# Kernel tuning notes

Hardware: AMD Instinct MI355X
Metric: run time of the kernel (lower is better)

The kernel has to match this reference:

```python
import jax, jax.numpy as jnp
import numpy as np

NUM_ROWS = 4096      # out_features
GROUP_COUNT = 32
GROUP_SIZE = 128     # in_features = GROUP_COUNT * GROUP_SIZE = 4096
CODEBOOK_SIZE = 16   # 4-bit codes


def setup_inputs() -> dict:
    key = jax.random.key(0)
    k1, k2, k3, k4 = jax.random.split(key, 4)
    x = jax.random.normal(k1, (2, 1024, GROUP_COUNT * GROUP_SIZE), dtype=jnp.float32)
    codebooks = jax.random.normal(k2, (NUM_ROWS, GROUP_COUNT, CODEBOOK_SIZE), dtype=jnp.float32)
    codes = jax.random.randint(k3, (NUM_ROWS, GROUP_COUNT, GROUP_SIZE), 0, CODEBOOK_SIZE, dtype=jnp.int32)
    bias = jax.random.normal(k4, (NUM_ROWS,), dtype=jnp.float32)
    return {"x": x, "codebooks": codebooks, "codes": codes, "bias": bias}


def _dequantize_weight(codes, codebooks):
    # codes: [R, G, S] int indices into last dim of codebooks [R, G, B]
    R, G, S = codes.shape
    W_hat = jnp.take_along_axis(codebooks, codes, axis=2)  # [R, G, S]
    return W_hat.reshape(R, G * S)  # [out_features, in_features]


def reference(x, codebooks, codes, bias):
    W = _dequantize_weight(codes, codebooks)           # [out, in]
    out = jnp.einsum("bsi,oi->bso", x, W) + bias       # F.linear
    return out
```

## Files before the change

kernel.cpp:

```cpp
#include <hip/hip_runtime.h>
#include <hip/hip_bf16.h>
#include <stdint.h>


#define M_DIM 2048
#define N_DIM 4096
#define K_DIM 4096

typedef __attribute__((ext_vector_type(4))) int i32x4;

__device__ __forceinline__ void async_load16(const void* g, void* l) {
    __builtin_amdgcn_global_load_lds(
        (const __attribute__((address_space(1))) uint32_t*)(uintptr_t)g,
        (__attribute__((address_space(3))) uint32_t*)(uint32_t)(uintptr_t)l,
        16, 0, 0);
}

__device__ __forceinline__ uint32_t pack4(int a, int b, int c, int d) {
    return (uint32_t)(a & 255) | ((uint32_t)(b & 255) << 8) |
           ((uint32_t)(c & 255) << 16) | ((uint32_t)(d & 255) << 24);
}

__device__ __forceinline__ int q8(float v, float inv) {
    return (int)rintf(v * inv);
}

__global__ __launch_bounds__(256) void prepass_q8(
    const float* __restrict__ cb,
    const int* __restrict__ codes,
    const float* __restrict__ x,
    uint32_t* __restrict__ wq,
    uint32_t* __restrict__ xq,
    float* __restrict__ sw,
    float* __restrict__ sx)
{
    __shared__ float scb[512];
    __shared__ float red[256];
    const int b = blockIdx.x, t = threadIdx.x;
    if (b < N_DIM) {
        const int o = b;
        const float c0 = cb[(size_t)o * 512 + t];
        const float c1 = cb[(size_t)o * 512 + 256 + t];
        scb[t] = c0; scb[t + 256] = c1;
        red[t] = fmaxf(fabsf(c0), fabsf(c1));
        __syncthreads();
        for (int s = 128; s > 0; s >>= 1) {
            if (t < s) red[t] = fmaxf(red[t], red[t + s]);
            __syncthreads();
        }
        const float amax = fmaxf(red[0], 1e-20f);
        const float inv = 127.0f / amax;
        if (t == 0) sw[o] = amax / 127.0f;
        const int* crow = codes + (size_t)o * K_DIM;
        uint32_t* orow = wq + (size_t)o * 1024;
#pragma unroll
        for (int i = 0; i < 4; ++i) {
            const int d = t + i * 256;
            const int4 c = *(const int4*)(crow + d * 4);
            const float* g = scb + (d >> 5) * 16;
            orow[d] = pack4(q8(g[c.x], inv), q8(g[c.y], inv),
                            q8(g[c.z], inv), q8(g[c.w], inv));
        }
    } else {
        const int m = b - N_DIM;
        const float* row = x + (size_t)m * K_DIM;
        float4 v[4];
        float am = 0.f;
#pragma unroll
        for (int i = 0; i < 4; ++i) {
            v[i] = *(const float4*)(row + (size_t)(t + i * 256) * 4);
            am = fmaxf(am, fmaxf(fmaxf(fabsf(v[i].x), fabsf(v[i].y)),
                                 fmaxf(fabsf(v[i].z), fabsf(v[i].w))));
        }
        red[t] = am;
        __syncthreads();
        for (int s = 128; s > 0; s >>= 1) {
            if (t < s) red[t] = fmaxf(red[t], red[t + s]);
            __syncthreads();
        }
        const float amax = fmaxf(red[0], 1e-20f);
        const float inv = 127.0f / amax;
        if (t == 0) sx[m] = amax / 127.0f;
        uint32_t* orow = xq + (size_t)m * 1024;
#pragma unroll
        for (int i = 0; i < 4; ++i)
            orow[t + i * 256] = pack4(q8(v[i].x, inv), q8(v[i].y, inv),
                                      q8(v[i].z, inv), q8(v[i].w, inv));
    }
}


__device__ __forceinline__ void compute_tile(
    const unsigned char* As, const unsigned char* Bs,
    const int wm, const int wn, const int l15, const int fs,
    i32x4 acc[8][4])
{
    i32x4 af[8], bf[4];
#pragma unroll
    for (int i = 0; i < 8; ++i)
        af[i] = *(const i32x4*)(As + (wm + i * 16 + l15) * 128 + fs);
#pragma unroll
    for (int i = 0; i < 4; ++i)
        bf[i] = *(const i32x4*)(Bs + (wn + i * 16 + l15) * 128 + fs);
#pragma unroll
    for (int mi = 0; mi < 8; ++mi)
#pragma unroll
        for (int ni = 0; ni < 4; ++ni)
            acc[mi][ni] = __builtin_amdgcn_mfma_i32_16x16x64_i8(
                af[mi], bf[ni], acc[mi][ni], 0, 0, 0);
}

__global__ __launch_bounds__(512, 2) void gemm_i8(
    const unsigned char* __restrict__ A,
    const unsigned char* __restrict__ B,
    const float* __restrict__ sx,
    const float* __restrict__ sw,
    const float* __restrict__ bias,
    float* __restrict__ C)
{
    __shared__ __align__(16) unsigned char smem[98304];
    unsigned char* As0 = smem;
    unsigned char* Bs0 = smem + 32768;
    unsigned char* As1 = smem + 49152;
    unsigned char* Bs1 = smem + 81920;

    const int tid  = threadIdx.x;
    const int w    = tid >> 6;
    const int lane = tid & 63;
    const int l15  = lane & 15;
    const int quad = lane >> 4;
    const int m0   = blockIdx.y * 256;
    const int n0   = blockIdx.x * 128;
    const int wk   = w >> 2;
    const int wm   = ((w >> 1) & 1) * 128;
    const int wn   = (w & 1) * 64;

    const int r8 = lane >> 3;
    const int sc = (lane & 7) ^ r8;
    const unsigned char* gA = A + (size_t)(m0 + w * 8 + r8) * K_DIM + sc * 16;
    const unsigned char* gB = B + (size_t)(n0 + w * 8 + r8) * K_DIM + sc * 16;

    const int fs = (((wk << 2) + quad) ^ (l15 & 7)) * 16;

    auto stage = [&](unsigned char* As, unsigned char* Bs, int k) {
        async_load16(gA + k,                        As +         w * 1024);
        async_load16(gA + k + (size_t)64  * K_DIM,  As + 8192  + w * 1024);
        async_load16(gA + k + (size_t)128 * K_DIM,  As + 16384 + w * 1024);
        async_load16(gA + k + (size_t)192 * K_DIM,  As + 24576 + w * 1024);
        async_load16(gB + k,                        Bs +         w * 1024);
        async_load16(gB + k + (size_t)64  * K_DIM,  Bs + 8192  + w * 1024);
    };

    i32x4 acc[8][4] = {};

    stage(As0, Bs0, 0);
    for (int k0 = 0; k0 < K_DIM; k0 += 256) {
        stage(As1, Bs1, k0 + 128);
        asm volatile("s_waitcnt vmcnt(6)" ::: "memory");
        __builtin_amdgcn_s_barrier();
        asm volatile("" ::: "memory");
        compute_tile(As0, Bs0, wm, wn, l15, fs, acc);
        asm volatile("s_waitcnt lgkmcnt(0)" ::: "memory");
        __builtin_amdgcn_sched_barrier(0);
        __builtin_amdgcn_s_barrier();

        if (k0 + 256 < K_DIM) {
            stage(As0, Bs0, k0 + 256);
            asm volatile("s_waitcnt vmcnt(6)" ::: "memory");
        } else {
            asm volatile("s_waitcnt vmcnt(0)" ::: "memory");
        }
        __builtin_amdgcn_s_barrier();
        asm volatile("" ::: "memory");
        compute_tile(As1, Bs1, wm, wn, l15, fs, acc);
        asm volatile("s_waitcnt lgkmcnt(0)" ::: "memory");
        __builtin_amdgcn_sched_barrier(0);
        __builtin_amdgcn_s_barrier();
    }

    i32x4* red = (i32x4*)smem;
    if (w == 4 || w == 5) {
        i32x4* dst = red + (w & 1) * 2048;
#pragma unroll
        for (int mi = 0; mi < 8; ++mi)
#pragma unroll
            for (int ni = 0; ni < 4; ++ni)
                dst[(mi * 4 + ni) * 64 + lane] = acc[mi][ni];
    }
    __syncthreads();
    if (w == 0 || w == 1) {
        const i32x4* src = red + (w & 1) * 2048;
#pragma unroll
        for (int mi = 0; mi < 8; ++mi)
#pragma unroll
            for (int ni = 0; ni < 4; ++ni) {
                const i32x4 v = src[(mi * 4 + ni) * 64 + lane];
                acc[mi][ni] = acc[mi][ni] + v;
            }
    }
    __syncthreads();
    if (w == 6 || w == 7) {
        i32x4* dst = red + (w & 1) * 2048;
#pragma unroll
        for (int mi = 0; mi < 8; ++mi)
#pragma unroll
            for (int ni = 0; ni < 4; ++ni)
                dst[(mi * 4 + ni) * 64 + lane] = acc[mi][ni];
    }
    __syncthreads();
    if (w == 2 || w == 3) {
        const i32x4* src = red + (w & 1) * 2048;
#pragma unroll
        for (int mi = 0; mi < 8; ++mi)
#pragma unroll
            for (int ni = 0; ni < 4; ++ni) {
                const i32x4 v = src[(mi * 4 + ni) * 64 + lane];
                acc[mi][ni] = acc[mi][ni] + v;
            }
    }

    if (w < 4) {
        float swv[4], bv[4];
#pragma unroll
        for (int ni = 0; ni < 4; ++ni) {
            const int col = n0 + wn + ni * 16 + l15;
            swv[ni] = sw[col];
            bv[ni]  = bias[col];
        }
#pragma unroll
        for (int mi = 0; mi < 8; ++mi) {
            float sxr[4];
#pragma unroll
            for (int r = 0; r < 4; ++r)
                sxr[r] = sx[m0 + wm + mi * 16 + quad * 4 + r];
#pragma unroll
            for (int ni = 0; ni < 4; ++ni) {
                const int col = n0 + wn + ni * 16 + l15;
                float* cp = C + (size_t)(m0 + wm + mi * 16 + quad * 4) * N_DIM + col;
#pragma unroll
                for (int r = 0; r < 4; ++r)
                    cp[(size_t)r * N_DIM] =
                        (float)acc[mi][ni][r] * (sxr[r] * swv[ni]) + bv[ni];
            }
        }
    }
}

__global__ __launch_bounds__(256) void naive_kernel(
    const float* __restrict__ x, const float* __restrict__ cb,
    const int* __restrict__ codes, const float* __restrict__ bias,
    float* __restrict__ out)
{
    const size_t idx = (size_t)blockIdx.x * 256 + threadIdx.x;
    const int n = (int)(idx & 4095);
    const int m = (int)(idx >> 12);
    const float* xr = x + (size_t)m * K_DIM;
    float s = bias[n];
    for (int g = 0; g < 32; ++g) {
        const float* cbr = cb + ((size_t)n * 32 + g) * 16;
        const int* cr = codes + ((size_t)n * 32 + g) * 128;
        const float* xg = xr + g * 128;
        for (int ss = 0; ss < 128; ++ss) s += xg[ss] * cbr[cr[ss]];
    }
    out[idx] = s;
}

extern "C" void kernel_launch(void* const* d_in, const int* in_sizes, int n_in,
                              void* d_out, int out_size, void* d_ws, size_t ws_size,
                              hipStream_t stream) {
    const float* x     = (const float*)d_in[0];
    const float* cb    = (const float*)d_in[1];
    const int*   codes = (const int*)d_in[2];
    const float* bias  = (const float*)d_in[3];
    float* out = (float*)d_out;

    const size_t szW = (size_t)N_DIM * K_DIM;
    const size_t szX = (size_t)M_DIM * K_DIM;
    const size_t need = szW + szX + (N_DIM + M_DIM) * sizeof(float);

    if (ws_size >= need) {
        unsigned char* Wq = (unsigned char*)d_ws;
        unsigned char* Xq = Wq + szW;
        float* sw = (float*)(Xq + szX);
        float* sx = sw + N_DIM;
        prepass_q8<<<dim3(N_DIM + M_DIM), dim3(256), 0, stream>>>(
            cb, codes, x, (uint32_t*)Wq, (uint32_t*)Xq, sw, sx);
        gemm_i8<<<dim3(N_DIM / 128, M_DIM / 256), dim3(512), 0, stream>>>(
            Xq, Wq, sx, sw, bias, out);
    } else {
        naive_kernel<<<dim3((M_DIM * N_DIM) / 256), dim3(256), 0, stream>>>(x, cb, codes, bias, out);
    }
}
```

Measured before the change: 173.8 us.

## Triple-buffer LDS and interleave async prefetch with half-tile MFMA phases

Replaces the double-buffered main loop with a three-stage LDS ring, prefetching two K-tiles ahead. Each K-tile is split into two MFMA halves: the A prefetch is issued between the first fragment loads and the first half, and the B prefetch before the second half. Barriers and s_setprio raise wave priority around the MFMA bursts. The goal is to hide global-load latency and spread the LDS-write traffic across the compute instead of issuing it in one burst. The cost is extra LDS (144KB), more barriers per tile, and tighter wait-count bookkeeping.

```diff
diff --git a/kernel.cpp b/kernel.cpp
--- a/kernel.cpp
+++ b/kernel.cpp
@@ -90,24 +90,60 @@
 }
 
 
-__device__ __forceinline__ void compute_tile(
-    const unsigned char* As, const unsigned char* Bs,
-    const int wm, const int wn, const int l15, const int fs,
-    i32x4 acc[8][4])
+template <bool STAGE, int VM>
+__device__ __forceinline__ void ktile(
+    const unsigned char* As_c, const unsigned char* Bs_c,
+    unsigned char* As_p, unsigned char* Bs_p, int kpre,
+    const unsigned char* gA, const unsigned char* gB,
+    int wm, int wn, int l15, int fs, int w, i32x4 acc[8][4])
 {
-    i32x4 af[8], bf[4];
-#pragma unroll
-    for (int i = 0; i < 8; ++i)
-        af[i] = *(const i32x4*)(As + (wm + i * 16 + l15) * 128 + fs);
+    i32x4 af[4], bf[4];
 #pragma unroll
     for (int i = 0; i < 4; ++i)
-        bf[i] = *(const i32x4*)(Bs + (wn + i * 16 + l15) * 128 + fs);
-#pragma unroll
-    for (int mi = 0; mi < 8; ++mi)
+        af[i] = *(const i32x4*)(As_c + (wm + i * 16 + l15) * 128 + fs);
+#pragma unroll
+    for (int i = 0; i < 4; ++i)
+        bf[i] = *(const i32x4*)(Bs_c + (wn + i * 16 + l15) * 128 + fs);
+    if (STAGE) {
+        async_load16(gA + kpre,                         As_p +         w * 1024);
+        async_load16(gA + kpre + (size_t)64  * K_DIM,   As_p + 8192  + w * 1024);
+        async_load16(gA + kpre + (size_t)128 * K_DIM,   As_p + 16384 + w * 1024);
+        async_load16(gA + kpre + (size_t)192 * K_DIM,   As_p + 24576 + w * 1024);
+    }
+    asm volatile("" ::: "memory");
+    __builtin_amdgcn_s_barrier();
+    __builtin_amdgcn_s_setprio(1);
+#pragma unroll
+    for (int mi = 0; mi < 4; ++mi)
 #pragma unroll
         for (int ni = 0; ni < 4; ++ni)
             acc[mi][ni] = __builtin_amdgcn_mfma_i32_16x16x64_i8(
                 af[mi], bf[ni], acc[mi][ni], 0, 0, 0);
+    __builtin_amdgcn_s_setprio(0);
+    asm volatile("" ::: "memory");
+    __builtin_amdgcn_s_barrier();
+
+#pragma unroll
+    for (int i = 0; i < 4; ++i)
+        af[i] = *(const i32x4*)(As_c + (wm + 64 + i * 16 + l15) * 128 + fs);
+    if (STAGE) {
+        async_load16(gB + kpre,                         Bs_p +        w * 1024);
+        async_load16(gB + kpre + (size_t)64 * K_DIM,    Bs_p + 8192 + w * 1024);
+    }
+    asm volatile("" ::: "memory");
+    __builtin_amdgcn_s_barrier();
+    __builtin_amdgcn_s_setprio(1);
+#pragma unroll
+    for (int mi = 0; mi < 4; ++mi)
+#pragma unroll
+        for (int ni = 0; ni < 4; ++ni)
+            acc[4 + mi][ni] = __builtin_amdgcn_mfma_i32_16x16x64_i8(
+                af[mi], bf[ni], acc[4 + mi][ni], 0, 0, 0);
+    __builtin_amdgcn_s_setprio(0);
+    if (VM == 6)      asm volatile("s_waitcnt vmcnt(6)" ::: "memory");
+    else if (VM == 0) asm volatile("s_waitcnt vmcnt(0)" ::: "memory");
+    asm volatile("" ::: "memory");
+    __builtin_amdgcn_s_barrier();
 }
 
 __global__ __launch_bounds__(512, 2) void gemm_i8(
@@ -118,11 +154,13 @@
     const float* __restrict__ bias,
     float* __restrict__ C)
 {
-    __shared__ __align__(16) unsigned char smem[98304];
+    __shared__ __align__(16) unsigned char smem[147456];
     unsigned char* As0 = smem;
     unsigned char* Bs0 = smem + 32768;
     unsigned char* As1 = smem + 49152;
     unsigned char* Bs1 = smem + 81920;
+    unsigned char* As2 = smem + 98304;
+    unsigned char* Bs2 = smem + 131072;
 
     const int tid  = threadIdx.x;
     const int w    = tid >> 6;
@@ -142,41 +180,37 @@
 
     const int fs = (((wk << 2) + quad) ^ (l15 & 7)) * 16;
 
-    auto stage = [&](unsigned char* As, unsigned char* Bs, int k) {
-        async_load16(gA + k,                        As +         w * 1024);
-        async_load16(gA + k + (size_t)64  * K_DIM,  As + 8192  + w * 1024);
-        async_load16(gA + k + (size_t)128 * K_DIM,  As + 16384 + w * 1024);
-        async_load16(gA + k + (size_t)192 * K_DIM,  As + 24576 + w * 1024);
-        async_load16(gB + k,                        Bs +         w * 1024);
-        async_load16(gB + k + (size_t)64  * K_DIM,  Bs + 8192  + w * 1024);
-    };
-
     i32x4 acc[8][4] = {};
 
-    stage(As0, Bs0, 0);
-    for (int k0 = 0; k0 < K_DIM; k0 += 256) {
-        stage(As1, Bs1, k0 + 128);
-        asm volatile("s_waitcnt vmcnt(6)" ::: "memory");
-        __builtin_amdgcn_s_barrier();
-        asm volatile("" ::: "memory");
-        compute_tile(As0, Bs0, wm, wn, l15, fs, acc);
-        asm volatile("s_waitcnt lgkmcnt(0)" ::: "memory");
-        __builtin_amdgcn_sched_barrier(0);
-        __builtin_amdgcn_s_barrier();
-
-        if (k0 + 256 < K_DIM) {
-            stage(As0, Bs0, k0 + 256);
-            asm volatile("s_waitcnt vmcnt(6)" ::: "memory");
-        } else {
-            asm volatile("s_waitcnt vmcnt(0)" ::: "memory");
-        }
-        __builtin_amdgcn_s_barrier();
-        asm volatile("" ::: "memory");
-        compute_tile(As1, Bs1, wm, wn, l15, fs, acc);
-        asm volatile("s_waitcnt lgkmcnt(0)" ::: "memory");
-        __builtin_amdgcn_sched_barrier(0);
-        __builtin_amdgcn_s_barrier();
-    }
+    {
+        async_load16(gA,                          As0 +         w * 1024);
+        async_load16(gA + (size_t)64  * K_DIM,    As0 + 8192  + w * 1024);
+        async_load16(gA + (size_t)128 * K_DIM,    As0 + 16384 + w * 1024);
+        async_load16(gA + (size_t)192 * K_DIM,    As0 + 24576 + w * 1024);
+        async_load16(gB,                          Bs0 +        w * 1024);
+        async_load16(gB + (size_t)64 * K_DIM,     Bs0 + 8192 + w * 1024);
+        async_load16(gA + 128,                        As1 +         w * 1024);
+        async_load16(gA + 128 + (size_t)64  * K_DIM,  As1 + 8192  + w * 1024);
+        async_load16(gA + 128 + (size_t)128 * K_DIM,  As1 + 16384 + w * 1024);
+        async_load16(gA + 128 + (size_t)192 * K_DIM,  As1 + 24576 + w * 1024);
+        async_load16(gB + 128,                        Bs1 +        w * 1024);
+        async_load16(gB + 128 + (size_t)64 * K_DIM,   Bs1 + 8192 + w * 1024);
+    }
+    asm volatile("s_waitcnt vmcnt(6)" ::: "memory");
+    asm volatile("" ::: "memory");
+    __builtin_amdgcn_s_barrier();
+
+    for (int it = 0; it < 10; ++it) {
+        const int t = it * 3;
+        ktile<true, 6>(As0, Bs0, As2, Bs2, (t + 2) * 128,
+                       gA, gB, wm, wn, l15, fs, w, acc);
+        ktile<true, 6>(As1, Bs1, As0, Bs0, (t + 3) * 128,
+                       gA, gB, wm, wn, l15, fs, w, acc);
+        ktile<true, 6>(As2, Bs2, As1, Bs1, (t + 4) * 128,
+                       gA, gB, wm, wn, l15, fs, w, acc);
+    }
+    ktile<false, 0>(As0, Bs0, As1, Bs1, 0, gA, gB, wm, wn, l15, fs, w, acc);
+    ktile<false, -1>(As1, Bs1, As2, Bs2, 0, gA, gB, wm, wn, l15, fs, w, acc);
 
     i32x4* red = (i32x4*)smem;
     if (w == 4 || w == 5) {
```

New measurement: 170.5 us. About the same (-1.9%).

## Pre-swizzle quantized operands into MFMA fragment order and load directly to registers

Applied to the files above, without the earlier changes.

The quantization prepass now writes int8 weights and activations in a tiled layout that matches the MFMA fragment order, one 16-byte vector per lane per K-tile. The GEMM drops its LDS staging (async global-to-LDS loads, barriers, double-buffered shared tiles) and instead loads fragments straight from global memory into registers, with register double buffering across K-tiles. This removes LDS traffic and barrier synchronisation. In exchange, operand reuse across waves now relies on cache hits in L2/L1 rather than shared memory, and more registers are needed for the two fragment buffers.

```diff
diff --git a/kernel.cpp b/kernel.cpp
--- a/kernel.cpp
+++ b/kernel.cpp
@@ -8,13 +8,6 @@
 #define K_DIM 4096
 
 typedef __attribute__((ext_vector_type(4))) int i32x4;
-
-__device__ __forceinline__ void async_load16(const void* g, void* l) {
-    __builtin_amdgcn_global_load_lds(
-        (const __attribute__((address_space(1))) uint32_t*)(uintptr_t)g,
-        (__attribute__((address_space(3))) uint32_t*)(uint32_t)(uintptr_t)l,
-        16, 0, 0);
-}
 
 __device__ __forceinline__ uint32_t pack4(int a, int b, int c, int d) {
     return (uint32_t)(a & 255) | ((uint32_t)(b & 255) << 8) |
@@ -29,14 +22,16 @@
     const float* __restrict__ cb,
     const int* __restrict__ codes,
     const float* __restrict__ x,
-    uint32_t* __restrict__ wq,
-    uint32_t* __restrict__ xq,
+    uint4* __restrict__ wq,
+    uint4* __restrict__ xq,
     float* __restrict__ sw,
     float* __restrict__ sx)
 {
     __shared__ float scb[512];
     __shared__ float red[256];
     const int b = blockIdx.x, t = threadIdx.x;
+    const int c  = t;
+    const int kt = c >> 3, wkc = (c >> 2) & 1, qd = c & 3;
     if (b < N_DIM) {
         const int o = b;
         const float c0 = cb[(size_t)o * 512 + t];
@@ -51,26 +46,31 @@
         const float amax = fmaxf(red[0], 1e-20f);
         const float inv = 127.0f / amax;
         if (t == 0) sw[o] = amax / 127.0f;
-        const int* crow = codes + (size_t)o * K_DIM;
-        uint32_t* orow = wq + (size_t)o * 1024;
-#pragma unroll
-        for (int i = 0; i < 4; ++i) {
-            const int d = t + i * 256;
-            const int4 c = *(const int4*)(crow + d * 4);
-            const float* g = scb + (d >> 5) * 16;
-            orow[d] = pack4(q8(g[c.x], inv), q8(g[c.y], inv),
-                            q8(g[c.z], inv), q8(g[c.w], inv));
-        }
+        const int4* crow = (const int4*)(codes + (size_t)o * K_DIM);
+        const int4 i0 = crow[c * 4 + 0];
+        const int4 i1 = crow[c * 4 + 1];
+        const int4 i2 = crow[c * 4 + 2];
+        const int4 i3 = crow[c * 4 + 3];
+        const float* g = scb + (c >> 3) * 16;
+        uint4 ov;
+        ov.x = pack4(q8(g[i0.x], inv), q8(g[i0.y], inv), q8(g[i0.z], inv), q8(g[i0.w], inv));
+        ov.y = pack4(q8(g[i1.x], inv), q8(g[i1.y], inv), q8(g[i1.z], inv), q8(g[i1.w], inv));
+        ov.z = pack4(q8(g[i2.x], inv), q8(g[i2.y], inv), q8(g[i2.z], inv), q8(g[i2.w], inv));
+        ov.w = pack4(q8(g[i3.x], inv), q8(g[i3.y], inv), q8(g[i3.z], inv), q8(g[i3.w], inv));
+        const int nt = o >> 7, wn2 = (o >> 6) & 1, ir = (o >> 4) & 3, l15 = o & 15;
+        const size_t idx = ((size_t)(nt * 32 + kt) * 16 + (wn2 * 2 + wkc) * 4 + ir) * 64
+                           + qd * 16 + l15;
+        wq[idx] = ov;
     } else {
         const int m = b - N_DIM;
-        const float* row = x + (size_t)m * K_DIM;
+        const float4* row = (const float4*)(x + (size_t)m * K_DIM);
         float4 v[4];
         float am = 0.f;
 #pragma unroll
-        for (int i = 0; i < 4; ++i) {
-            v[i] = *(const float4*)(row + (size_t)(t + i * 256) * 4);
-            am = fmaxf(am, fmaxf(fmaxf(fabsf(v[i].x), fabsf(v[i].y)),
-                                 fmaxf(fabsf(v[i].z), fabsf(v[i].w))));
+        for (int j = 0; j < 4; ++j) {
+            v[j] = row[c * 4 + j];
+            am = fmaxf(am, fmaxf(fmaxf(fabsf(v[j].x), fabsf(v[j].y)),
+                                 fmaxf(fabsf(v[j].z), fabsf(v[j].w))));
         }
         red[t] = am;
         __syncthreads();
@@ -81,102 +81,81 @@
         const float amax = fmaxf(red[0], 1e-20f);
         const float inv = 127.0f / amax;
         if (t == 0) sx[m] = amax / 127.0f;
-        uint32_t* orow = xq + (size_t)m * 1024;
-#pragma unroll
-        for (int i = 0; i < 4; ++i)
-            orow[t + i * 256] = pack4(q8(v[i].x, inv), q8(v[i].y, inv),
-                                      q8(v[i].z, inv), q8(v[i].w, inv));
-    }
-}
-
-
-__device__ __forceinline__ void compute_tile(
-    const unsigned char* As, const unsigned char* Bs,
-    const int wm, const int wn, const int l15, const int fs,
-    i32x4 acc[8][4])
-{
-    i32x4 af[8], bf[4];
-#pragma unroll
-    for (int i = 0; i < 8; ++i)
-        af[i] = *(const i32x4*)(As + (wm + i * 16 + l15) * 128 + fs);
-#pragma unroll
-    for (int i = 0; i < 4; ++i)
-        bf[i] = *(const i32x4*)(Bs + (wn + i * 16 + l15) * 128 + fs);
+        uint4 ov;
+        ov.x = pack4(q8(v[0].x, inv), q8(v[0].y, inv), q8(v[0].z, inv), q8(v[0].w, inv));
+        ov.y = pack4(q8(v[1].x, inv), q8(v[1].y, inv), q8(v[1].z, inv), q8(v[1].w, inv));
+        ov.z = pack4(q8(v[2].x, inv), q8(v[2].y, inv), q8(v[2].z, inv), q8(v[2].w, inv));
+        ov.w = pack4(q8(v[3].x, inv), q8(v[3].y, inv), q8(v[3].z, inv), q8(v[3].w, inv));
+        const int mt = m >> 8, wm2 = (m >> 7) & 1, ir = (m >> 4) & 7, l15 = m & 15;
+        const size_t idx = ((size_t)(mt * 32 + kt) * 32 + (wm2 * 2 + wkc) * 8 + ir) * 64
+                           + qd * 16 + l15;
+        xq[idx] = ov;
+    }
+}
+
+
+__device__ __forceinline__ void load_frags(
+    const i32x4* __restrict__ pA, const i32x4* __restrict__ pB,
+    int kt, i32x4 a[8], i32x4 b[4])
+{
+#pragma unroll
+    for (int i = 0; i < 8; ++i) a[i] = pA[(size_t)kt * 2048 + i * 64];
+#pragma unroll
+    for (int i = 0; i < 4; ++i) b[i] = pB[(size_t)kt * 1024 + i * 64];
+}
+
+__device__ __forceinline__ void mfma_tile(
+    const i32x4 a[8], const i32x4 b[4], i32x4 acc[8][4])
+{
 #pragma unroll
     for (int mi = 0; mi < 8; ++mi)
 #pragma unroll
         for (int ni = 0; ni < 4; ++ni)
             acc[mi][ni] = __builtin_amdgcn_mfma_i32_16x16x64_i8(
-                af[mi], bf[ni], acc[mi][ni], 0, 0, 0);
+                a[mi], b[ni], acc[mi][ni], 0, 0, 0);
 }
 
 __global__ __launch_bounds__(512, 2) void gemm_i8(
-    const unsigned char* __restrict__ A,
-    const unsigned char* __restrict__ B,
+    const i32x4* __restrict__ A,
+    const i32x4* __restrict__ B,
     const float* __restrict__ sx,
     const float* __restrict__ sw,
     const float* __restrict__ bias,
     float* __restrict__ C)
 {
-    __shared__ __align__(16) unsigned char smem[98304];
-    unsigned char* As0 = smem;
-    unsigned char* Bs0 = smem + 32768;
-    unsigned char* As1 = smem + 49152;
-    unsigned char* Bs1 = smem + 81920;
+    __shared__ __align__(16) unsigned char smem[65536];
 
     const int tid  = threadIdx.x;
     const int w    = tid >> 6;
     const int lane = tid & 63;
     const int l15  = lane & 15;
     const int quad = lane >> 4;
-    const int m0   = blockIdx.y * 256;
-    const int n0   = blockIdx.x * 128;
+    const int nt   = blockIdx.x;
+    const int mt   = blockIdx.y;
+    const int m0   = mt * 256;
+    const int n0   = nt * 128;
     const int wk   = w >> 2;
-    const int wm   = ((w >> 1) & 1) * 128;
-    const int wn   = (w & 1) * 64;
-
-    const int r8 = lane >> 3;
-    const int sc = (lane & 7) ^ r8;
-    const unsigned char* gA = A + (size_t)(m0 + w * 8 + r8) * K_DIM + sc * 16;
-    const unsigned char* gB = B + (size_t)(n0 + w * 8 + r8) * K_DIM + sc * 16;
-
-    const int fs = (((wk << 2) + quad) ^ (l15 & 7)) * 16;
-
-    auto stage = [&](unsigned char* As, unsigned char* Bs, int k) {
-        async_load16(gA + k,                        As +         w * 1024);
-        async_load16(gA + k + (size_t)64  * K_DIM,  As + 8192  + w * 1024);
-        async_load16(gA + k + (size_t)128 * K_DIM,  As + 16384 + w * 1024);
-        async_load16(gA + k + (size_t)192 * K_DIM,  As + 24576 + w * 1024);
-        async_load16(gB + k,                        Bs +         w * 1024);
-        async_load16(gB + k + (size_t)64  * K_DIM,  Bs + 8192  + w * 1024);
-    };
+    const int wm2  = (w >> 1) & 1;
+    const int wn2  = w & 1;
+    const int wm   = wm2 * 128;
+    const int wn   = wn2 * 64;
+
+    const i32x4* pA = A + (size_t)mt * 65536 + (size_t)(wm2 * 2 + wk) * 512 + lane;
+    const i32x4* pB = B + (size_t)nt * 32768 + (size_t)(wn2 * 2 + wk) * 256 + lane;
 
     i32x4 acc[8][4] = {};
-
-    stage(As0, Bs0, 0);
-    for (int k0 = 0; k0 < K_DIM; k0 += 256) {
-        stage(As1, Bs1, k0 + 128);
-        asm volatile("s_waitcnt vmcnt(6)" ::: "memory");
-        __builtin_amdgcn_s_barrier();
-        asm volatile("" ::: "memory");
-        compute_tile(As0, Bs0, wm, wn, l15, fs, acc);
-        asm volatile("s_waitcnt lgkmcnt(0)" ::: "memory");
-        __builtin_amdgcn_sched_barrier(0);
-        __builtin_amdgcn_s_barrier();
-
-        if (k0 + 256 < K_DIM) {
-            stage(As0, Bs0, k0 + 256);
-            asm volatile("s_waitcnt vmcnt(6)" ::: "memory");
-        } else {
-            asm volatile("s_waitcnt vmcnt(0)" ::: "memory");
-        }
-        __builtin_amdgcn_s_barrier();
-        asm volatile("" ::: "memory");
-        compute_tile(As1, Bs1, wm, wn, l15, fs, acc);
-        asm volatile("s_waitcnt lgkmcnt(0)" ::: "memory");
-        __builtin_amdgcn_sched_barrier(0);
-        __builtin_amdgcn_s_barrier();
-    }
+    i32x4 aA[8], bA[4], aB[8], bB[4];
+
+    load_frags(pA, pB, 0, aA, bA);
+    for (int kt = 0; kt < 30; kt += 2) {
+        load_frags(pA, pB, kt + 1, aB, bB);
+        mfma_tile(aA, bA, acc);
+        load_frags(pA, pB, kt + 2, aA, bA);
+        mfma_tile(aB, bB, acc);
+    }
+    load_frags(pA, pB, 31, aB, bB);
+    mfma_tile(aA, bA, acc);
+    mfma_tile(aB, bB, acc);
 
     i32x4* red = (i32x4*)smem;
     if (w == 4 || w == 5) {
@@ -284,9 +263,9 @@
         float* sw = (float*)(Xq + szX);
         float* sx = sw + N_DIM;
         prepass_q8<<<dim3(N_DIM + M_DIM), dim3(256), 0, stream>>>(
-            cb, codes, x, (uint32_t*)Wq, (uint32_t*)Xq, sw, sx);
+            cb, codes, x, (uint4*)Wq, (uint4*)Xq, sw, sx);
         gemm_i8<<<dim3(N_DIM / 128, M_DIM / 256), dim3(512), 0, stream>>>(
-            Xq, Wq, sx, sw, bias, out);
+            (const i32x4*)Xq, (const i32x4*)Wq, sx, sw, bias, out);
     } else {
         naive_kernel<<<dim3((M_DIM * N_DIM) / 256), dim3(256), 0, stream>>>(x, cb, codes, bias, out);
     }
```

After: 195.5 us. 12.5% more time.
